# Kernel optimization log

Hardware: AMD Instinct MI355X
Metric: run time of the kernel (lower is better)

## Reference

```python
import jax, jax.numpy as jnp
import numpy as np

HIDDEN = 1024
MOE_INTER = 512
SHARED_INTER = 2048
N_EXPERTS = 32
TOP_K = 6
N_GROUP = 8
TOPK_GROUP = 4
ROUTED_SCALE = 2.5


def setup_inputs() -> dict:
    key = jax.random.key(0)
    ks = jax.random.split(key, 6)
    s = 0.02
    return {
        "hidden_states": jax.random.normal(ks[0], (2, 1024, HIDDEN), jnp.float32),
        "gate_w": jax.random.normal(ks[1], (N_EXPERTS, HIDDEN), jnp.float32) * s,
        "e_bias": jnp.zeros((N_EXPERTS,), jnp.float32),  # e_score_correction_bias (non-trainable)
        "up_w": jax.random.normal(ks[2], (N_EXPERTS, MOE_INTER, HIDDEN), jnp.float32) * s,
        "down_w": jax.random.normal(ks[3], (N_EXPERTS, HIDDEN, MOE_INTER), jnp.float32) * s,
        "shared_up_w": jax.random.normal(ks[4], (SHARED_INTER, HIDDEN), jnp.float32) * s,
        "shared_down_w": jax.random.normal(ks[5], (HIDDEN, SHARED_INTER), jnp.float32) * s,
    }


def _relu2(x):
    # Nemotron-H 'relu2' activation: relu(x)^2
    return jnp.square(jax.nn.relu(x))


def _router(x, gate_w, e_bias):
    # x: [T, H] -> topk_idx [T, K] (int), topk_w [T, K] (fp32)
    T = x.shape[0]
    logits = x.astype(jnp.float32) @ gate_w.astype(jnp.float32).T  # [T, E]
    scores = jax.nn.sigmoid(logits)
    sc = scores + e_bias[None, :]
    # group-limited routing: top-2 sum per group, keep topk_group groups
    g = sc.reshape(T, N_GROUP, N_EXPERTS // N_GROUP)
    group_scores = jax.lax.top_k(g, 2)[0].sum(-1)                  # [T, G]
    group_idx = jax.lax.top_k(group_scores, TOPK_GROUP)[1]         # [T, TG]
    group_mask = jnp.zeros_like(group_scores).at[jnp.arange(T)[:, None], group_idx].set(1.0)
    score_mask = jnp.repeat(group_mask, N_EXPERTS // N_GROUP, axis=1)  # [T, E]
    masked = jnp.where(score_mask > 0, sc, 0.0)
    topk_idx = jax.lax.stop_gradient(jax.lax.top_k(masked, TOP_K)[1])  # torch path is @no_grad
    topk_w = jnp.take_along_axis(scores, topk_idx, axis=1)         # gather from unbiased scores
    topk_w = topk_w / (topk_w.sum(-1, keepdims=True) + 1e-20)      # norm_topk_prob
    topk_w = topk_w * ROUTED_SCALE
    return topk_idx, topk_w


def reference(hidden_states, gate_w, e_bias, up_w, down_w, shared_up_w, shared_down_w):
    B, S, H = hidden_states.shape
    x = hidden_states.reshape(-1, H)  # [T, H]
    T = x.shape[0]
    topk_idx, topk_w = _router(x, gate_w, e_bias)
    # combine weights as dense [T, E] (scatter of top-k weights)
    combine = jnp.zeros((T, N_EXPERTS), topk_w.dtype).at[jnp.arange(T)[:, None], topk_idx].add(topk_w)
    # dense-masked expert compute; weight applied on intermediate (equivalent since
    # down_proj is linear with no bias): out = sum_e w_te * down_e(act(up_e(x)))
    h = _relu2(jnp.einsum('th,eih->tei', x, up_w))   # [T, E, I]
    h = h * combine[:, :, None]
    moe_out = jnp.einsum('tei,ehi->th', h, down_w)   # [T, H]
    shared = _relu2(x @ shared_up_w.T) @ shared_down_w.T
    return (moe_out + shared).reshape(B, S, H)


if __name__ == "__main__":
    out = reference(**setup_inputs())
    print(out.shape, out.dtype)
```

## Files before the change

kernel.cpp:

```cpp
#include <hip/hip_runtime.h>

typedef unsigned short u16;
typedef __bf16 bf16x8 __attribute__((ext_vector_type(8)));
typedef float f32x4 __attribute__((ext_vector_type(4)));

#define T_TOK 2048
#define HID   1024
#define NEXP  32
#define IM    512
#define SI    2048
#define TOPK  6
#define PLAN_MAX 160

__device__ __forceinline__ u16 f2bf(float f){
  unsigned u = __float_as_uint(f);
  u += 0x7FFFu + ((u >> 16) & 1u);
  return (u16)(u >> 16);
}

__device__ __forceinline__ void gll16(const void* g, void* l){
  __builtin_amdgcn_global_load_lds((const __attribute__((address_space(1))) void*)g,
                                   (__attribute__((address_space(3))) void*)l, 16, 0, 0);
}

__global__ __launch_bounds__(256) void cvt_all_kernel(const float4* __restrict__ s0,
                                                      const float4* __restrict__ s1,
                                                      const float4* __restrict__ s2,
                                                      const float4* __restrict__ s3,
                                                      const float4* __restrict__ s4,
                                                      ushort4* __restrict__ d0,
                                                      ushort4* __restrict__ d1,
                                                      ushort4* __restrict__ d2,
                                                      ushort4* __restrict__ d3,
                                                      ushort4* __restrict__ d4){
  long i = (long)blockIdx.x * 256 + threadIdx.x;
  const float4* s; ushort4* d;
  if      (i <  524288L)                 { s = s0;            d = d0;            }
  else if (i <  524288L + 4194304L)      { s = s1 - 524288L;  d = d1 - 524288L;  }
  else if (i <  524288L + 8388608L)      { s = s2 - 4718592L; d = d2 - 4718592L; }
  else if (i <  524288L + 8912896L)      { s = s3 - 8912896L; d = d3 - 8912896L; }
  else                                   { s = s4 - 9437184L; d = d4 - 9437184L; }
  float4 v = s[i];
  ushort4 o; o.x = f2bf(v.x); o.y = f2bf(v.y); o.z = f2bf(v.z); o.w = f2bf(v.w);
  d[i] = o;
}

__global__ __launch_bounds__(256) void router_kernel(const float* __restrict__ x,
                                                     const float* __restrict__ gate,
                                                     const float* __restrict__ ebias,
                                                     int* __restrict__ ce,
                                                     float* __restrict__ cw){
  int wave = threadIdx.x >> 6;
  int lane = threadIdx.x & 63;
  int t = blockIdx.x * 4 + wave;
  int e = lane & 31, half = lane >> 5;
  const float4* xv = (const float4*)(x + (size_t)t * HID);
  const float4* gv = (const float4*)(gate + (size_t)e * HID);
  double d0 = 0, d1 = 0, d2 = 0, d3 = 0;
  for (int i = half * 128; i < half * 128 + 128; i++){
    float4 a = xv[i], b = gv[i];
    d0 += (double)a.x * b.x; d1 += (double)a.y * b.y;
    d2 += (double)a.z * b.z; d3 += (double)a.w * b.w;
  }
  double acc = (d0 + d1) + (d2 + d3);
  acc += __shfl_xor(acc, 32);
  double score = 1.0 / (1.0 + exp(-acc));
  double sc = score + (double)ebias[e];
  double o1  = __shfl_xor(sc, 1);
  double hi  = fmax(sc, o1), lo = fmin(sc, o1);
  double ohi = __shfl_xor(hi, 2), olo = __shfl_xor(lo, 2);
  double gs  = (hi >= ohi) ? hi + fmax(lo, ohi) : ohi + fmax(olo, hi);
  int g = e >> 2;
  int rank = 0;
#pragma unroll
  for (int j = 0; j < 8; j++){
    double gj = __shfl(gs, j * 4);
    if (gj > gs || (gj == gs && j < g)) rank++;
  }
  double cur = (rank < 4) ? sc : 0.0;
  int sel_e[TOPK]; double sel_w[TOPK]; double wsum = 0.0;
#pragma unroll
  for (int k = 0; k < TOPK; k++){
    double bv = cur; int bi = lane;
#pragma unroll
    for (int m = 32; m >= 1; m >>= 1){
      double ov = __shfl_xor(bv, m); int oi = __shfl_xor(bi, m);
      if (ov > bv || (ov == bv && oi < bi)) { bv = ov; bi = oi; }
    }
    if ((bi & 31) == e) cur = -1e300;
    double ws = __shfl(score, bi);
    sel_e[k] = bi; sel_w[k] = ws; wsum += ws;
  }
  double scale = 2.5 / (wsum + 1e-20);
#pragma unroll
  for (int k = 0; k < TOPK; k++){
    if (lane == k){
      ce[t * TOPK + k] = sel_e[k] & 31;
      cw[t * TOPK + k] = (float)(sel_w[k] * scale);
    }
  }
}

__global__ __launch_bounds__(256) void build_kernel(const int* __restrict__ ce,
                                                    const float* __restrict__ cw,
                                                    int* __restrict__ cnt,
                                                    int* __restrict__ tok,
                                                    float* __restrict__ wl){
  int e = blockIdx.x;
  int tid = threadIdx.x, lane = tid & 63, wave = tid >> 6;
  __shared__ int wsum[4];
  int running = 0;
  for (int base = 0; base < T_TOK * TOPK; base += 256){
    int i = base + tid;
    bool m = (ce[i] == e);
    unsigned long long bal = __ballot(m);
    int woff = __popcll(bal & ((1ull << lane) - 1ull));
    if (lane == 0) wsum[wave] = __popcll(bal);
    __syncthreads();
    int wbase = 0;
#pragma unroll
    for (int wv = 0; wv < 4; wv++) if (wv < wave) wbase += wsum[wv];
    int btot = wsum[0] + wsum[1] + wsum[2] + wsum[3];
    if (m){
      int t = i / TOPK, k = i - t * TOPK;
      int pos = running + wbase + woff;
      tok[e * T_TOK + pos] = (t << 3) | k;
      wl[e * T_TOK + pos] = cw[i];
    }
    running += btot;
    __syncthreads();
  }
  if (tid == 0) cnt[e] = running;
}

__global__ __launch_bounds__(256) void plan_kernel(const int* __restrict__ cnt,
                                                   int* __restrict__ plan){
  int tid = threadIdx.x;
  if (tid < PLAN_MAX) plan[1 + tid] = -1;
  __syncthreads();
  if (tid == 0){
    int n = 0;
    for (int e = 0; e < NEXP; e++){
      int c = cnt[e];
      for (int tb = 0; tb < c; tb += 128) plan[1 + n++] = (tb << 8) | e;
    }
    plan[0] = n;
  }
}

__device__ __forceinline__ void gemm_core(
    const char* gA0, const char* gA1, const char* gB0, const char* gB1,
    u16* lA, u16* lB, int iters, int tid, int wrow, int wcol, int quad, int l16,
    f32x4 acc[4][4])
{
  char* dA0 = (char*)lA + tid*16;
  char* dA1 = (char*)lA + 4096 + tid*16;
  char* dB0 = (char*)lB + tid*16;
  char* dB1 = (char*)lB + 4096 + tid*16;
  for (int it = 0; it < iters; ++it){
    gll16(gA0, dA0); gll16(gA1, dA1);
    gll16(gB0, dB0); gll16(gB1, dB1);
    gA0 += 64; gA1 += 64; gB0 += 64; gB1 += 64;
    __syncthreads();
    bf16x8 af[4], bfr[4];
#pragma unroll
    for (int mt = 0; mt < 4; mt++) af[mt] = *(const bf16x8*)&lA[(wrow + mt*16 + l16)*32 + quad*8];
#pragma unroll
    for (int nt = 0; nt < 4; nt++) bfr[nt] = *(const bf16x8*)&lB[(wcol + nt*16 + l16)*32 + quad*8];
#pragma unroll
    for (int mt = 0; mt < 4; mt++)
#pragma unroll
      for (int nt = 0; nt < 4; nt++)
        acc[mt][nt] = __builtin_amdgcn_mfma_f32_16x16x32_bf16(af[mt], bfr[nt], acc[mt][nt], 0, 0, 0);
    __syncthreads();
  }
}

#define ACC_INIT f32x4 acc[4][4]; \
  _Pragma("unroll") for (int i_ = 0; i_ < 4; i_++) \
  _Pragma("unroll") for (int j_ = 0; j_ < 4; j_++) acc[i_][j_] = (f32x4){0.f,0.f,0.f,0.f};

__global__ __launch_bounds__(256) void sh_up_kernel(const u16* __restrict__ A,
                                                    const u16* __restrict__ B,
                                                    u16* __restrict__ C){
  __shared__ u16 lA[128*32], lB[128*32];
  int tid = threadIdx.x;
  int bm = blockIdx.x*128, bn = blockIdx.y*128;
  int lane = tid & 63, wave = tid >> 6, quad = lane >> 4, l16 = lane & 15;
  int wrow = (wave >> 1)*64, wcol = (wave & 1)*64;
  int srow = tid >> 2, sseg = (tid & 3)*16;
  const char* gA0 = (const char*)(A + (size_t)(bm + srow)*HID) + sseg;
  const char* gA1 = (const char*)(A + (size_t)(bm + 64 + srow)*HID) + sseg;
  const char* gB0 = (const char*)(B + (size_t)(bn + srow)*HID) + sseg;
  const char* gB1 = (const char*)(B + (size_t)(bn + 64 + srow)*HID) + sseg;
  ACC_INIT;
  gemm_core(gA0, gA1, gB0, gB1, lA, lB, HID/32, tid, wrow, wcol, quad, l16, acc);
#pragma unroll
  for (int mt = 0; mt < 4; mt++)
#pragma unroll
    for (int nt = 0; nt < 4; nt++)
#pragma unroll
      for (int r = 0; r < 4; r++){
        int m = bm + wrow + mt*16 + quad*4 + r;
        int n = bn + wcol + nt*16 + l16;
        float v = acc[mt][nt][r]; v = fmaxf(v, 0.f); v *= v;
        C[(size_t)m*SI + n] = f2bf(v);
      }
}

__global__ __launch_bounds__(256) void sh_down_kernel(const u16* __restrict__ A,
                                                      const u16* __restrict__ B,
                                                      float* __restrict__ C){
  __shared__ u16 lA[128*32], lB[128*32];
  int tid = threadIdx.x;
  int bm = blockIdx.x*128, bn = blockIdx.y*128;
  int lane = tid & 63, wave = tid >> 6, quad = lane >> 4, l16 = lane & 15;
  int wrow = (wave >> 1)*64, wcol = (wave & 1)*64;
  int srow = tid >> 2, sseg = (tid & 3)*16;
  const char* gA0 = (const char*)(A + (size_t)(bm + srow)*SI) + sseg;
  const char* gA1 = (const char*)(A + (size_t)(bm + 64 + srow)*SI) + sseg;
  const char* gB0 = (const char*)(B + (size_t)(bn + srow)*SI) + sseg;
  const char* gB1 = (const char*)(B + (size_t)(bn + 64 + srow)*SI) + sseg;
  ACC_INIT;
  gemm_core(gA0, gA1, gB0, gB1, lA, lB, SI/32, tid, wrow, wcol, quad, l16, acc);
#pragma unroll
  for (int mt = 0; mt < 4; mt++)
#pragma unroll
    for (int nt = 0; nt < 4; nt++)
#pragma unroll
      for (int r = 0; r < 4; r++){
        int m = bm + wrow + mt*16 + quad*4 + r;
        int n = bn + wcol + nt*16 + l16;
        C[(size_t)m*HID + n] = acc[mt][nt][r];
      }
}

__global__ __launch_bounds__(256) void expert_up_kernel(const u16* __restrict__ xb,
                                                        const u16* __restrict__ upb,
                                                        const int* __restrict__ cnt,
                                                        const int* __restrict__ tok,
                                                        const float* __restrict__ wl,
                                                        const int* __restrict__ plan,
                                                        u16* __restrict__ hws){
  int pv = plan[1 + blockIdx.x];
  if (pv < 0) return;
  int e = pv & 255;
  int tb = pv >> 8;
  int c = cnt[e];
  int bn = blockIdx.y * 128;
  const int* tl = tok + e * T_TOK;
  const float* wle = wl + e * T_TOK;
  __shared__ u16 lA[128*32], lB[128*32];
  int tid = threadIdx.x;
  int lane = tid & 63, wave = tid >> 6, quad = lane >> 4, l16 = lane & 15;
  int wrow = (wave >> 1)*64, wcol = (wave & 1)*64;
  int srow = tid >> 2, sseg = (tid & 3)*16;
  int s0 = tb + srow;      if (s0 > c-1) s0 = c-1;
  int s1 = tb + 64 + srow; if (s1 > c-1) s1 = c-1;
  int t0 = tl[s0] >> 3, t1 = tl[s1] >> 3;
  const char* gA0 = (const char*)(xb + (size_t)t0*HID) + sseg;
  const char* gA1 = (const char*)(xb + (size_t)t1*HID) + sseg;
  const u16* Bb = upb + (size_t)e * IM * HID;
  const char* gB0 = (const char*)(Bb + (size_t)(bn + srow)*HID) + sseg;
  const char* gB1 = (const char*)(Bb + (size_t)(bn + 64 + srow)*HID) + sseg;
  ACC_INIT;
  gemm_core(gA0, gA1, gB0, gB1, lA, lB, HID/32, tid, wrow, wcol, quad, l16, acc);
#pragma unroll
  for (int mt = 0; mt < 4; mt++)
#pragma unroll
    for (int r = 0; r < 4; r++){
      int s = tb + wrow + mt*16 + quad*4 + r;
      if (s < c){
        int code = tl[s];
        float w = wle[s];
        size_t hb = ((size_t)(code >> 3) * TOPK + (code & 7)) * IM;
#pragma unroll
        for (int nt = 0; nt < 4; nt++){
          float v = acc[mt][nt][r]; v = fmaxf(v, 0.f); v = v * v * w;
          hws[hb + bn + wcol + nt*16 + l16] = f2bf(v);
        }
      }
    }
}

__global__ __launch_bounds__(256) void expert_down_kernel(const u16* __restrict__ hws,
                                                          const u16* __restrict__ dnb,
                                                          const int* __restrict__ cnt,
                                                          const int* __restrict__ tok,
                                                          const int* __restrict__ plan,
                                                          float* __restrict__ dws){
  int pv = plan[1 + blockIdx.x];
  if (pv < 0) return;
  int e = pv & 255;
  int tb = pv >> 8;
  int c = cnt[e];
  int bn = blockIdx.y * 128;
  const int* tl = tok + e * T_TOK;
  __shared__ u16 lA[128*32], lB[128*32];
  int tid = threadIdx.x;
  int lane = tid & 63, wave = tid >> 6, quad = lane >> 4, l16 = lane & 15;
  int wrow = (wave >> 1)*64, wcol = (wave & 1)*64;
  int srow = tid >> 2, sseg = (tid & 3)*16;
  int s0 = tb + srow;      if (s0 > c-1) s0 = c-1;
  int s1 = tb + 64 + srow; if (s1 > c-1) s1 = c-1;
  int c0 = tl[s0], c1 = tl[s1];
  const char* gA0 = (const char*)(hws + ((size_t)(c0 >> 3)*TOPK + (c0 & 7))*IM) + sseg;
  const char* gA1 = (const char*)(hws + ((size_t)(c1 >> 3)*TOPK + (c1 & 7))*IM) + sseg;
  const u16* Bb = dnb + (size_t)e * HID * IM;
  const char* gB0 = (const char*)(Bb + (size_t)(bn + srow)*IM) + sseg;
  const char* gB1 = (const char*)(Bb + (size_t)(bn + 64 + srow)*IM) + sseg;
  ACC_INIT;
  gemm_core(gA0, gA1, gB0, gB1, lA, lB, IM/32, tid, wrow, wcol, quad, l16, acc);
#pragma unroll
  for (int mt = 0; mt < 4; mt++)
#pragma unroll
    for (int r = 0; r < 4; r++){
      int s = tb + wrow + mt*16 + quad*4 + r;
      if (s < c){
        int code = tl[s];
        size_t db = ((size_t)(code >> 3) * TOPK + (code & 7)) * HID;
#pragma unroll
        for (int nt = 0; nt < 4; nt++)
          dws[db + bn + wcol + nt*16 + l16] = acc[mt][nt][r];
      }
    }
}

__global__ __launch_bounds__(256) void reduce_kernel(const float4* __restrict__ dws,
                                                     float4* __restrict__ out){
  int i = blockIdx.x * 256 + threadIdx.x;
  int t = i >> 8;
  int col = i & 255;
  const float4* p = dws + (size_t)t * TOPK * 256 + col;
  float4 s = out[i];
#pragma unroll
  for (int k = 0; k < TOPK; k++){
    float4 v = p[(size_t)k * 256];
    s.x += v.x; s.y += v.y; s.z += v.z; s.w += v.w;
  }
  out[i] = s;
}

extern "C" void kernel_launch(void* const* d_in, const int* in_sizes, int n_in,
                              void* d_out, int out_size, void* d_ws, size_t ws_size,
                              hipStream_t stream) {
  const float* x    = (const float*)d_in[0];
  const float* gate = (const float*)d_in[1];
  const float* eb   = (const float*)d_in[2];
  const float* upw  = (const float*)d_in[3];
  const float* dnw  = (const float*)d_in[4];
  const float* supw = (const float*)d_in[5];
  const float* sdnw = (const float*)d_in[6];
  float* out = (float*)d_out;

  char* w = (char*)d_ws;
  size_t o = 0;
  int*   cnt  = (int*)(w + o);   o += 1024;
  int*   plan = (int*)(w + o);   o += 1024;
  int*   ce   = (int*)(w + o);   o += (size_t)T_TOK * TOPK * 4;
  float* cw   = (float*)(w + o); o += (size_t)T_TOK * TOPK * 4;
  int*   tok  = (int*)(w + o);   o += (size_t)NEXP * T_TOK * 4;
  float* wl   = (float*)(w + o); o += (size_t)NEXP * T_TOK * 4;
  u16*   xb   = (u16*)(w + o);   o += (size_t)T_TOK * HID * 2;
  u16*   dnb  = (u16*)(w + o);   o += (size_t)NEXP * HID * IM * 2;
  u16*   hws  = (u16*)(w + o);   o += (size_t)T_TOK * TOPK * IM * 2;
  size_t region = o;
  u16*   upb  = (u16*)(w + o);   o += (size_t)NEXP * IM * HID * 2;
  u16*   supb = (u16*)(w + o);   o += (size_t)SI * HID * 2;
  u16*   sdnb = (u16*)(w + o);   o += (size_t)HID * SI * 2;
  u16*   shh  = (u16*)(w + o);   o += (size_t)T_TOK * SI * 2;
  float* dws  = (float*)(w + region);

  cvt_all_kernel<<<9961472 / 256, 256, 0, stream>>>(
      (const float4*)x, (const float4*)upw, (const float4*)dnw,
      (const float4*)supw, (const float4*)sdnw,
      (ushort4*)xb, (ushort4*)upb, (ushort4*)dnb, (ushort4*)supb, (ushort4*)sdnb);

  router_kernel<<<T_TOK/4, 256, 0, stream>>>(x, gate, eb, ce, cw);
  build_kernel<<<NEXP, 256, 0, stream>>>(ce, cw, cnt, tok, wl);
  plan_kernel<<<1, 256, 0, stream>>>(cnt, plan);

  sh_up_kernel<<<dim3(T_TOK/128, SI/128), 256, 0, stream>>>(xb, supb, shh);
  sh_down_kernel<<<dim3(T_TOK/128, HID/128), 256, 0, stream>>>(shh, sdnb, out);

  expert_up_kernel<<<dim3(PLAN_MAX, IM/128), 256, 0, stream>>>(xb, upb, cnt, tok, wl, plan, hws);
  expert_down_kernel<<<dim3(PLAN_MAX, HID/128), 256, 0, stream>>>(hws, dnb, cnt, tok, plan, dws);

  reduce_kernel<<<(T_TOK * HID / 4) / 256, 256, 0, stream>>>((const float4*)dws, (float4*)out);
}
```

Baseline: 391.6 us.

## Merge conversion with router and shared-up with expert-up into combined launches

The fp32-to-bf16 conversion and the router are folded into one launch, with blocks split by index, and each conversion thread now handles two float4 elements. The shared-expert up GEMM and the routed-expert up GEMM are merged into one launch over a flat grid, so the two independent workloads can fill the GPU together and launch gaps shrink. The cost is extra branching per block, plus possible imbalance from mixing conversion blocks with router blocks.

```diff
diff --git a/kernel.cpp b/kernel.cpp
--- a/kernel.cpp
+++ b/kernel.cpp
@@ -11,6 +11,7 @@
 #define SI    2048
 #define TOPK  6
 #define PLAN_MAX 160
+#define CVT_BLOCKS 19456
 
 __device__ __forceinline__ u16 f2bf(float f){
   unsigned u = __float_as_uint(f);
@@ -23,46 +24,54 @@
                                    (__attribute__((address_space(3))) void*)l, 16, 0, 0);
 }
 
-__global__ __launch_bounds__(256) void cvt_all_kernel(const float4* __restrict__ s0,
-                                                      const float4* __restrict__ s1,
-                                                      const float4* __restrict__ s2,
-                                                      const float4* __restrict__ s3,
-                                                      const float4* __restrict__ s4,
-                                                      ushort4* __restrict__ d0,
-                                                      ushort4* __restrict__ d1,
-                                                      ushort4* __restrict__ d2,
-                                                      ushort4* __restrict__ d3,
-                                                      ushort4* __restrict__ d4){
-  long i = (long)blockIdx.x * 256 + threadIdx.x;
-  const float4* s; ushort4* d;
-  if      (i <  524288L)                 { s = s0;            d = d0;            }
-  else if (i <  524288L + 4194304L)      { s = s1 - 524288L;  d = d1 - 524288L;  }
-  else if (i <  524288L + 8388608L)      { s = s2 - 4718592L; d = d2 - 4718592L; }
-  else if (i <  524288L + 8912896L)      { s = s3 - 8912896L; d = d3 - 8912896L; }
-  else                                   { s = s4 - 9437184L; d = d4 - 9437184L; }
-  float4 v = s[i];
+__device__ __forceinline__ ushort4 cvt4(float4 v){
   ushort4 o; o.x = f2bf(v.x); o.y = f2bf(v.y); o.z = f2bf(v.z); o.w = f2bf(v.w);
-  d[i] = o;
-}
-
-__global__ __launch_bounds__(256) void router_kernel(const float* __restrict__ x,
+  return o;
+}
+
+__global__ __launch_bounds__(256) void phase1_kernel(const float4* __restrict__ s0,
+                                                     const float4* __restrict__ s1,
+                                                     const float4* __restrict__ s2,
+                                                     const float4* __restrict__ s3,
+                                                     const float4* __restrict__ s4,
+                                                     ushort4* __restrict__ d0,
+                                                     ushort4* __restrict__ d1,
+                                                     ushort4* __restrict__ d2,
+                                                     ushort4* __restrict__ d3,
+                                                     ushort4* __restrict__ d4,
                                                      const float* __restrict__ gate,
                                                      const float* __restrict__ ebias,
                                                      int* __restrict__ ce,
                                                      float* __restrict__ cw){
-  int wave = threadIdx.x >> 6;
-  int lane = threadIdx.x & 63;
-  int t = blockIdx.x * 4 + wave;
+  int tid = threadIdx.x;
+  if (blockIdx.x < CVT_BLOCKS){
+    long i = (long)blockIdx.x * 512 + tid;
+    const float4* s; ushort4* d;
+    if      (i <  524288L) { s = s0;            d = d0;            }
+    else if (i < 4718592L) { s = s1 - 524288L;  d = d1 - 524288L;  }
+    else if (i < 8912896L) { s = s2 - 4718592L; d = d2 - 4718592L; }
+    else if (i < 9437184L) { s = s3 - 8912896L; d = d3 - 8912896L; }
+    else                   { s = s4 - 9437184L; d = d4 - 9437184L; }
+    float4 v0 = s[i];
+    float4 v1 = s[i + 256];
+    d[i]       = cvt4(v0);
+    d[i + 256] = cvt4(v1);
+    return;
+  }
+  const float* x = (const float*)s0;
+  int wave = tid >> 6;
+  int lane = tid & 63;
+  int t = (blockIdx.x - CVT_BLOCKS) * 4 + wave;
   int e = lane & 31, half = lane >> 5;
   const float4* xv = (const float4*)(x + (size_t)t * HID);
   const float4* gv = (const float4*)(gate + (size_t)e * HID);
-  double d0 = 0, d1 = 0, d2 = 0, d3 = 0;
+  double p0 = 0, p1 = 0, p2 = 0, p3 = 0;
   for (int i = half * 128; i < half * 128 + 128; i++){
     float4 a = xv[i], b = gv[i];
-    d0 += (double)a.x * b.x; d1 += (double)a.y * b.y;
-    d2 += (double)a.z * b.z; d3 += (double)a.w * b.w;
-  }
-  double acc = (d0 + d1) + (d2 + d3);
+    p0 += (double)a.x * b.x; p1 += (double)a.y * b.y;
+    p2 += (double)a.z * b.z; p3 += (double)a.w * b.w;
+  }
+  double acc = (p0 + p1) + (p2 + p3);
   acc += __shfl_xor(acc, 32);
   double score = 1.0 / (1.0 + exp(-acc));
   double sc = score + (double)ebias[e];
@@ -180,32 +189,77 @@
   _Pragma("unroll") for (int i_ = 0; i_ < 4; i_++) \
   _Pragma("unroll") for (int j_ = 0; j_ < 4; j_++) acc[i_][j_] = (f32x4){0.f,0.f,0.f,0.f};
 
-__global__ __launch_bounds__(256) void sh_up_kernel(const u16* __restrict__ A,
-                                                    const u16* __restrict__ B,
-                                                    u16* __restrict__ C){
+__global__ __launch_bounds__(256) void up_kernel(const u16* __restrict__ xb,
+                                                 const u16* __restrict__ supb,
+                                                 const u16* __restrict__ upb,
+                                                 const int* __restrict__ cnt,
+                                                 const int* __restrict__ tok,
+                                                 const float* __restrict__ wl,
+                                                 const int* __restrict__ plan,
+                                                 u16* __restrict__ shh,
+                                                 u16* __restrict__ hws){
   __shared__ u16 lA[128*32], lB[128*32];
   int tid = threadIdx.x;
-  int bm = blockIdx.x*128, bn = blockIdx.y*128;
   int lane = tid & 63, wave = tid >> 6, quad = lane >> 4, l16 = lane & 15;
   int wrow = (wave >> 1)*64, wcol = (wave & 1)*64;
   int srow = tid >> 2, sseg = (tid & 3)*16;
-  const char* gA0 = (const char*)(A + (size_t)(bm + srow)*HID) + sseg;
-  const char* gA1 = (const char*)(A + (size_t)(bm + 64 + srow)*HID) + sseg;
-  const char* gB0 = (const char*)(B + (size_t)(bn + srow)*HID) + sseg;
-  const char* gB1 = (const char*)(B + (size_t)(bn + 64 + srow)*HID) + sseg;
+
+  if (blockIdx.x < 256){
+    int bm = (blockIdx.x >> 4)*128, bn = (blockIdx.x & 15)*128;
+    const char* gA0 = (const char*)(xb + (size_t)(bm + srow)*HID) + sseg;
+    const char* gA1 = (const char*)(xb + (size_t)(bm + 64 + srow)*HID) + sseg;
+    const char* gB0 = (const char*)(supb + (size_t)(bn + srow)*HID) + sseg;
+    const char* gB1 = (const char*)(supb + (size_t)(bn + 64 + srow)*HID) + sseg;
+    ACC_INIT;
+    gemm_core(gA0, gA1, gB0, gB1, lA, lB, HID/32, tid, wrow, wcol, quad, l16, acc);
+#pragma unroll
+    for (int mt = 0; mt < 4; mt++)
+#pragma unroll
+      for (int nt = 0; nt < 4; nt++)
+#pragma unroll
+        for (int r = 0; r < 4; r++){
+          int m = bm + wrow + mt*16 + quad*4 + r;
+          int n = bn + wcol + nt*16 + l16;
+          float v = acc[mt][nt][r]; v = fmaxf(v, 0.f); v *= v;
+          shh[(size_t)m*SI + n] = f2bf(v);
+        }
+    return;
+  }
+  int idx = blockIdx.x - 256;
+  int pv = plan[1 + (idx >> 2)];
+  if (pv < 0) return;
+  int e = pv & 255;
+  int tb = pv >> 8;
+  int c = cnt[e];
+  int bn = (idx & 3) * 128;
+  const int* tl = tok + e * T_TOK;
+  const float* wle = wl + e * T_TOK;
+  int s0 = tb + srow;      if (s0 > c-1) s0 = c-1;
+  int s1 = tb + 64 + srow; if (s1 > c-1) s1 = c-1;
+  int t0 = tl[s0] >> 3, t1 = tl[s1] >> 3;
+  const char* gA0 = (const char*)(xb + (size_t)t0*HID) + sseg;
+  const char* gA1 = (const char*)(xb + (size_t)t1*HID) + sseg;
+  const u16* Bb = upb + (size_t)e * IM * HID;
+  const char* gB0 = (const char*)(Bb + (size_t)(bn + srow)*HID) + sseg;
+  const char* gB1 = (const char*)(Bb + (size_t)(bn + 64 + srow)*HID) + sseg;
   ACC_INIT;
   gemm_core(gA0, gA1, gB0, gB1, lA, lB, HID/32, tid, wrow, wcol, quad, l16, acc);
 #pragma unroll
   for (int mt = 0; mt < 4; mt++)
 #pragma unroll
-    for (int nt = 0; nt < 4; nt++)
-#pragma unroll
-      for (int r = 0; r < 4; r++){
-        int m = bm + wrow + mt*16 + quad*4 + r;
-        int n = bn + wcol + nt*16 + l16;
-        float v = acc[mt][nt][r]; v = fmaxf(v, 0.f); v *= v;
-        C[(size_t)m*SI + n] = f2bf(v);
+    for (int r = 0; r < 4; r++){
+      int s = tb + wrow + mt*16 + quad*4 + r;
+      if (s < c){
+        int code = tl[s];
+        float w = wle[s];
+        size_t hb = ((size_t)(code >> 3) * TOPK + (code & 7)) * IM;
+#pragma unroll
+        for (int nt = 0; nt < 4; nt++){
+          float v = acc[mt][nt][r]; v = fmaxf(v, 0.f); v = v * v * w;
+          hws[hb + bn + (wcol + nt*16 + l16)] = f2bf(v);
+        }
       }
+    }
 }
 
 __global__ __launch_bounds__(256) void sh_down_kernel(const u16* __restrict__ A,
@@ -233,54 +287,6 @@
         int n = bn + wcol + nt*16 + l16;
         C[(size_t)m*HID + n] = acc[mt][nt][r];
       }
-}
-
-__global__ __launch_bounds__(256) void expert_up_kernel(const u16* __restrict__ xb,
-                                                        const u16* __restrict__ upb,
-                                                        const int* __restrict__ cnt,
-                                                        const int* __restrict__ tok,
-                                                        const float* __restrict__ wl,
-                                                        const int* __restrict__ plan,
-                                                        u16* __restrict__ hws){
-  int pv = plan[1 + blockIdx.x];
-  if (pv < 0) return;
-  int e = pv & 255;
-  int tb = pv >> 8;
-  int c = cnt[e];
-  int bn = blockIdx.y * 128;
-  const int* tl = tok + e * T_TOK;
-  const float* wle = wl + e * T_TOK;
-  __shared__ u16 lA[128*32], lB[128*32];
-  int tid = threadIdx.x;
-  int lane = tid & 63, wave = tid >> 6, quad = lane >> 4, l16 = lane & 15;
-  int wrow = (wave >> 1)*64, wcol = (wave & 1)*64;
-  int srow = tid >> 2, sseg = (tid & 3)*16;
-  int s0 = tb + srow;      if (s0 > c-1) s0 = c-1;
-  int s1 = tb + 64 + srow; if (s1 > c-1) s1 = c-1;
-  int t0 = tl[s0] >> 3, t1 = tl[s1] >> 3;
-  const char* gA0 = (const char*)(xb + (size_t)t0*HID) + sseg;
-  const char* gA1 = (const char*)(xb + (size_t)t1*HID) + sseg;
-  const u16* Bb = upb + (size_t)e * IM * HID;
-  const char* gB0 = (const char*)(Bb + (size_t)(bn + srow)*HID) + sseg;
-  const char* gB1 = (const char*)(Bb + (size_t)(bn + 64 + srow)*HID) + sseg;
-  ACC_INIT;
-  gemm_core(gA0, gA1, gB0, gB1, lA, lB, HID/32, tid, wrow, wcol, quad, l16, acc);
-#pragma unroll
-  for (int mt = 0; mt < 4; mt++)
-#pragma unroll
-    for (int r = 0; r < 4; r++){
-      int s = tb + wrow + mt*16 + quad*4 + r;
-      if (s < c){
-        int code = tl[s];
-        float w = wle[s];
-        size_t hb = ((size_t)(code >> 3) * TOPK + (code & 7)) * IM;
-#pragma unroll
-        for (int nt = 0; nt < 4; nt++){
-          float v = acc[mt][nt][r]; v = fmaxf(v, 0.f); v = v * v * w;
-          hws[hb + bn + wcol + nt*16 + l16] = f2bf(v);
-        }
-      }
-    }
 }
 
 __global__ __launch_bounds__(256) void expert_down_kernel(const u16* __restrict__ hws,
@@ -321,7 +327,7 @@
         size_t db = ((size_t)(code >> 3) * TOPK + (code & 7)) * HID;
 #pragma unroll
         for (int nt = 0; nt < 4; nt++)
-          dws[db + bn + wcol + nt*16 + l16] = acc[mt][nt][r];
+          dws[db + bn + (wcol + nt*16 + l16)] = acc[mt][nt][r];
       }
     }
 }
@@ -357,33 +363,32 @@
   size_t o = 0;
   int*   cnt  = (int*)(w + o);   o += 1024;
   int*   plan = (int*)(w + o);   o += 1024;
-  int*   ce   = (int*)(w + o);   o += (size_t)T_TOK * TOPK * 4;
-  float* cw   = (float*)(w + o); o += (size_t)T_TOK * TOPK * 4;
-  int*   tok  = (int*)(w + o);   o += (size_t)NEXP * T_TOK * 4;
-  float* wl   = (float*)(w + o); o += (size_t)NEXP * T_TOK * 4;
-  u16*   xb   = (u16*)(w + o);   o += (size_t)T_TOK * HID * 2;
-  u16*   dnb  = (u16*)(w + o);   o += (size_t)NEXP * HID * IM * 2;
-  u16*   hws  = (u16*)(w + o);   o += (size_t)T_TOK * TOPK * IM * 2;
+  int*   ce   = (int*)(w + o);   o += 49152;
+  float* cw   = (float*)(w + o); o += 49152;
+  int*   tok  = (int*)(w + o);   o += 262144;
+  float* wl   = (float*)(w + o); o += 262144;
+  u16*   xb   = (u16*)(w + o);   o += 4194304;
+  u16*   dnb  = (u16*)(w + o);   o += 33554432;
+  u16*   hws  = (u16*)(w + o);   o += 12582912;
   size_t region = o;
-  u16*   upb  = (u16*)(w + o);   o += (size_t)NEXP * IM * HID * 2;
-  u16*   supb = (u16*)(w + o);   o += (size_t)SI * HID * 2;
-  u16*   sdnb = (u16*)(w + o);   o += (size_t)HID * SI * 2;
-  u16*   shh  = (u16*)(w + o);   o += (size_t)T_TOK * SI * 2;
+  u16*   upb  = (u16*)(w + o);   o += 33554432;
+  u16*   supb = (u16*)(w + o);   o += 4194304;
+  u16*   sdnb = (u16*)(w + o);   o += 4194304;
+  u16*   shh  = (u16*)(w + o);   o += 8388608;
   float* dws  = (float*)(w + region);
 
-  cvt_all_kernel<<<9961472 / 256, 256, 0, stream>>>(
+  phase1_kernel<<<CVT_BLOCKS + T_TOK/4, 256, 0, stream>>>(
       (const float4*)x, (const float4*)upw, (const float4*)dnw,
       (const float4*)supw, (const float4*)sdnw,
-      (ushort4*)xb, (ushort4*)upb, (ushort4*)dnb, (ushort4*)supb, (ushort4*)sdnb);
-
-  router_kernel<<<T_TOK/4, 256, 0, stream>>>(x, gate, eb, ce, cw);
+      (ushort4*)xb, (ushort4*)upb, (ushort4*)dnb, (ushort4*)supb, (ushort4*)sdnb,
+      gate, eb, ce, cw);
+
   build_kernel<<<NEXP, 256, 0, stream>>>(ce, cw, cnt, tok, wl);
   plan_kernel<<<1, 256, 0, stream>>>(cnt, plan);
 
-  sh_up_kernel<<<dim3(T_TOK/128, SI/128), 256, 0, stream>>>(xb, supb, shh);
+  up_kernel<<<256 + PLAN_MAX*4, 256, 0, stream>>>(xb, supb, upb, cnt, tok, wl, plan, shh, hws);
+
   sh_down_kernel<<<dim3(T_TOK/128, HID/128), 256, 0, stream>>>(shh, sdnb, out);
-
-  expert_up_kernel<<<dim3(PLAN_MAX, IM/128), 256, 0, stream>>>(xb, upb, cnt, tok, wl, plan, hws);
   expert_down_kernel<<<dim3(PLAN_MAX, HID/128), 256, 0, stream>>>(hws, dnb, cnt, tok, plan, dws);
 
   reduce_kernel<<<(T_TOK * HID / 4) / 256, 256, 0, stream>>>((const float4*)dws, (float4*)out);
```

New measurement: 415.7 us. 1.06x slower.
